# Kernel optimization log

Hardware: AMD Instinct MI355X
Metric: run time of the kernel (lower is better)

## Reference

```python
import jax, jax.numpy as jnp
import numpy as np

DQ = 256  # query feature size
DK = 256  # key feature size
DV = 256  # value feature size
B, SQ, SK = 4, 256, 256
D = DQ + DK  # MLP hidden width (512)


def setup_inputs() -> dict:
    key = jax.random.key(0)
    ks = jax.random.split(key, 7)
    Q = jax.random.normal(ks[0], (B, SQ, DQ), dtype=jnp.float32)
    K = jax.random.normal(ks[1], (B, SK, DK), dtype=jnp.float32)
    V = jax.random.normal(ks[2], (B, SK, DV), dtype=jnp.float32)
    # key-padding style mask: True = masked out. Keep at least the first key
    # unmasked so softmax rows are well-behaved.
    mask_out = jax.random.randint(ks[3], (B, 1, SK), 0, 2).astype(jnp.bool_)
    mask_out = mask_out.at[:, :, 0].set(False)
    # nn.Linear(D, D, bias=True): weight [D, D], bias [D]
    lim1 = 1.0 / np.sqrt(D)
    W1 = jax.random.uniform(ks[4], (D, D), minval=-lim1, maxval=lim1, dtype=jnp.float32)
    b1 = jax.random.uniform(ks[5], (D,), minval=-lim1, maxval=lim1, dtype=jnp.float32)
    # nn.Linear(D, 1, bias=False): weight [1, D] -> store as vector [D]
    W2 = jax.random.uniform(ks[6], (D,), minval=-lim1, maxval=lim1, dtype=jnp.float32)
    return {"Q": Q, "K": K, "V": V, "mask_out": mask_out, "W1": W1, "b1": b1, "W2": W2}


def reference(Q, K, V, mask_out, W1, b1, W2):
    # Concat-then-Linear splits: cat([q,k]) @ W1.T == q @ W1[:, :DQ].T + k @ W1[:, DQ:].T
    q_h = jnp.einsum('bqd,hd->bqh', Q, W1[:, :DQ])          # [B,SQ,D]
    k_h = jnp.einsum('bkd,hd->bkh', K, W1[:, DQ:])          # [B,SK,D]
    hidden = q_h[:, :, None, :] + k_h[:, None, :, :] + b1   # [B,SQ,SK,D]
    act = jax.nn.leaky_relu(hidden, negative_slope=0.01)
    scores = jnp.einsum('bqkh,h->bqk', act, W2)             # [B,SQ,SK]
    scores = jnp.where(mask_out, jnp.float32(-1e9), scores)
    attn = jax.nn.softmax(scores, axis=-1)
    return jnp.einsum('bqk,bkv->bqv', attn, V)              # [B,SQ,DV]
```

## Files before the change

kernel.cpp:

```cpp
#include <hip/hip_runtime.h>

#define HH_OFF 0
#define KT_OFF (1024 * 512)

typedef short short8 __attribute__((ext_vector_type(8)));
typedef float f32x4 __attribute__((ext_vector_type(4)));

union S8 {
  short8 v;
  unsigned short s[8];
};

__device__ __forceinline__ unsigned bf16rne(float x) {
  unsigned u = __float_as_uint(x);
  u += 0x7FFFu + ((u >> 16) & 1u);
  return u >> 16;
}

__device__ __forceinline__ void cvt_split8(const float4& f0, const float4& f1,
                                           short8& hv8, short8& lv8) {
  float xs[8] = {f0.x, f0.y, f0.z, f0.w, f1.x, f1.y, f1.z, f1.w};
  S8 hv, lv;
#pragma unroll
  for (int e = 0; e < 8; ++e) {
    unsigned u = __float_as_uint(xs[e]);
    unsigned hu = u & 0xFFFF0000u;
    hv.s[e] = (unsigned short)(hu >> 16);
    float lo = xs[e] - __uint_as_float(hu);
    unsigned ul = __float_as_uint(lo);
    ul += 0x7FFFu + ((ul >> 16) & 1u);
    lv.s[e] = (unsigned short)(ul >> 16);
  }
  hv8 = hv.v;
  lv8 = lv.v;
}

__global__ __launch_bounds__(512) void gemm_k(const float* __restrict__ Q,
                                              const float* __restrict__ Kin,
                                              const float* __restrict__ W1,
                                              const float* __restrict__ b1,
                                              float* __restrict__ hh,
                                              unsigned* __restrict__ kT2) {
  __shared__ short AH[64 * 32], AL[64 * 32], BH[64 * 32], BL[64 * 32];
  const int t = threadIdx.x;
  const int blk = blockIdx.x;
  const bool isK = blk >= 128;
  const float *A, *B;
  int lda, ldb, m0, n0, aoff;
  if (!isK) {
    int bm = blk >> 3, bn = blk & 7;
    m0 = bm * 64; n0 = bn * 64;
    A = Q;   lda = 256; aoff = 0;
    B = W1;  ldb = 512;
  } else {
    int t2 = blk - 128;
    int bm = t2 >> 4, bn = t2 & 15;
    m0 = bm * 64; n0 = bn * 64;
    A = W1;  lda = 512; aoff = 256;
    B = Kin; ldb = 256;
  }
  const int mat = t >> 8;
  const int cc = t & 255;
  const int sr = cc >> 2;
  const int c8 = (cc & 3) * 8;
  const float* srcbase =
      mat ? (B + (size_t)(n0 + sr) * ldb + c8)
          : (A + (size_t)(m0 + sr) * lda + aoff + c8);
  short* dstH = (mat ? BH : AH) + sr * 32 + c8;
  short* dstL = (mat ? BL : AL) + sr * 32 + c8;

  const int w = t >> 6, lane = t & 63;
  const int wr = (w >> 2) * 32, wc = (w & 3) * 16;
  const int lane15 = lane & 15, lk8 = (lane >> 4) * 8;

  f32x4 acc[2] = {{0.f, 0.f, 0.f, 0.f}, {0.f, 0.f, 0.f, 0.f}};

  float4 f0 = *(const float4*)&srcbase[0];
  float4 f1 = *(const float4*)&srcbase[4];
  for (int ks = 0; ks < 8; ++ks) {
    short8 hv8, lv8;
    cvt_split8(f0, f1, hv8, lv8);
    __syncthreads();
    *(short8*)dstH = hv8;
    *(short8*)dstL = lv8;
    __syncthreads();
    if (ks < 7) {
      f0 = *(const float4*)&srcbase[(ks + 1) * 32];
      f1 = *(const float4*)&srcbase[(ks + 1) * 32 + 4];
    }
    short8 ah0 = *(const short8*)&AH[(wr + lane15) * 32 + lk8];
    short8 ah1 = *(const short8*)&AH[(wr + 16 + lane15) * 32 + lk8];
    short8 al0 = *(const short8*)&AL[(wr + lane15) * 32 + lk8];
    short8 al1 = *(const short8*)&AL[(wr + 16 + lane15) * 32 + lk8];
    short8 bh = *(const short8*)&BH[(wc + lane15) * 32 + lk8];
    short8 bl = *(const short8*)&BL[(wc + lane15) * 32 + lk8];
    acc[0] = __builtin_amdgcn_mfma_f32_16x16x32_bf16(ah0, bh, acc[0], 0, 0, 0);
    acc[1] = __builtin_amdgcn_mfma_f32_16x16x32_bf16(ah1, bh, acc[1], 0, 0, 0);
    acc[0] = __builtin_amdgcn_mfma_f32_16x16x32_bf16(ah0, bl, acc[0], 0, 0, 0);
    acc[1] = __builtin_amdgcn_mfma_f32_16x16x32_bf16(ah1, bl, acc[1], 0, 0, 0);
    acc[0] = __builtin_amdgcn_mfma_f32_16x16x32_bf16(al0, bh, acc[0], 0, 0, 0);
    acc[1] = __builtin_amdgcn_mfma_f32_16x16x32_bf16(al1, bh, acc[1], 0, 0, 0);
  }
  const int lg4 = (lane >> 4) * 4;
  if (!isK) {
#pragma unroll
    for (int i = 0; i < 2; ++i) {
#pragma unroll
      for (int reg = 0; reg < 4; ++reg) {
        int row = m0 + wr + i * 16 + lg4 + reg;
        hh[(size_t)row * 512 + n0 + wc + lane15] = acc[i][reg];
      }
    }
  } else {
    const int col = n0 + wc + lane15;
#pragma unroll
    for (int i = 0; i < 2; ++i) {
      int r0 = m0 + wr + i * 16 + lg4;
      float v0 = acc[i][0] + b1[r0 + 0];
      float v1 = acc[i][1] + b1[r0 + 1];
      float v2 = acc[i][2] + b1[r0 + 2];
      float v3 = acc[i][3] + b1[r0 + 3];
      unsigned p01 = bf16rne(v0) | (bf16rne(v1) << 16);
      unsigned p23 = bf16rne(v2) | (bf16rne(v3) << 16);
      int hp = r0 >> 1;
      kT2[(size_t)hp * 1024 + col] = p01;
      kT2[(size_t)(hp + 1) * 1024 + col] = p23;
    }
  }
}

__global__ __launch_bounds__(512) void attn_k(const float* __restrict__ hh,
                                              const unsigned* __restrict__ kT2,
                                              const float* __restrict__ V,
                                              const void* __restrict__ maskp,
                                              const float* __restrict__ W2,
                                              float* __restrict__ out) {
  __shared__ float smem[14016];
  __shared__ int sflag, nkS;
  __shared__ int wsumS[4];
  __shared__ int kidxS[256];
  float* att = smem;
  float* rowsum = smem + 1040;
  float* qlin = smem + 1044;
  float* qs = smem + 1056;
  float* w2s = smem + 3104;
  float* sabs = smem + 3616;
  float* klin = smem + 11936;
  float* red = smem + 3616;

  const int t = threadIdx.x;
  const int blk = blockIdx.x;
  const int b = blk >> 6;
  const int q4 = blk & 63;
  const int w = t >> 6, lane = t & 63;

  if (t == 0) sflag = 0;
  {
    const float* qbase = hh + (size_t)(b * 256 + q4 * 4) * 512;
    int row = t >> 7, c4 = (t & 127) * 4;
    *(float4*)&qs[row * 512 + c4] = *(const float4*)&qbase[(size_t)row * 512 + c4];
    if (t < 128) *(float4*)&w2s[t * 4] = *(const float4*)&W2[t * 4];
  }
  __syncthreads();
  if (t < 256) {
    const unsigned char* mb = (const unsigned char*)maskp;
    int nz = mb[t * 4 + 1] | mb[t * 4 + 2] | mb[t * 4 + 3];
    if (nz) atomicOr(&sflag, 1);
  }
  if (w < 4) {
    float p = 0.f;
#pragma unroll
    for (int u = 0; u < 8; ++u)
      p = fmaf(w2s[lane + 64 * u], qs[w * 512 + lane + 64 * u], p);
#pragma unroll
    for (int o = 32; o; o >>= 1) p += __shfl_xor(p, o, 64);
    if (lane == 0) qlin[w] = 0.505f * p;
  }
  __syncthreads();
  bool act = false;
  int pre = 0;
  if (t < 256) {
    const int flag = sflag;
    const unsigned char* m8 = (const unsigned char*)maskp;
    const int* m32 = (const int*)maskp;
    act = flag ? (m8[b * 256 + t] == 0) : (m32[b * 256 + t] == 0);
    unsigned long long bal = __ballot(act);
    pre = __popcll(bal & ((1ull << lane) - 1ull));
    if (lane == 0) wsumS[w] = __popcll(bal);
  }
  __syncthreads();
  if (t < 256 && act) {
    int off = 0;
#pragma unroll
    for (int ww = 0; ww < 4; ++ww)
      if (ww < w) off += wsumS[ww];
    kidxS[off + pre] = t;
  }
  if (t == 0) nkS = wsumS[0] + wsumS[1] + wsumS[2] + wsumS[3];
  __syncthreads();
  const int nk = nkS;
  const int ncg = (nk + 63) >> 6;

  {
    float sa[4][4] = {};
    float kl[4] = {};
    const unsigned* kTbase = kT2 + (size_t)b * 256;
    const unsigned* colp[4];
#pragma unroll
    for (int cg = 0; cg < 4; ++cg) {
      int ci = cg * 64 + lane;
      int kc = kidxS[ci < nk ? ci : (nk - 1)];
      colp[cg] = kTbase + kc;
    }
    const int hbase = w * 64;
#pragma unroll 2
    for (int hg = 0; hg < 16; ++hg) {
      const int h = hbase + hg * 4;
      const int hp = h >> 1;
      unsigned ua[4], ub[4];
#pragma unroll
      for (int cg = 0; cg < 4; ++cg)
        if (cg < ncg) {
          ua[cg] = colp[cg][(size_t)hp * 1024];
          ub[cg] = colp[cg][(size_t)(hp + 1) * 1024];
        }
      float w24[4], qv[4][4];
      *(float4*)w24 = *(const float4*)&w2s[h];
#pragma unroll
      for (int q = 0; q < 4; ++q)
        *(float4*)qv[q] = *(const float4*)&qs[q * 512 + h];
#pragma unroll
      for (int cg = 0; cg < 4; ++cg)
        if (cg < ncg) {
          float kv[4];
          kv[0] = __uint_as_float(ua[cg] << 16);
          kv[1] = __uint_as_float(ua[cg] & 0xFFFF0000u);
          kv[2] = __uint_as_float(ub[cg] << 16);
          kv[3] = __uint_as_float(ub[cg] & 0xFFFF0000u);
#pragma unroll
          for (int e = 0; e < 4; ++e) {
            kl[cg] = fmaf(w24[e], kv[e], kl[cg]);
#pragma unroll
            for (int q = 0; q < 4; ++q)
              sa[q][cg] = fmaf(w24[e], fabsf(qv[q][e] + kv[e]), sa[q][cg]);
          }
        }
    }
#pragma unroll
    for (int cg = 0; cg < 4; ++cg)
      if (cg < ncg) {
        int ci = cg * 64 + lane;
#pragma unroll
        for (int q = 0; q < 4; ++q) sabs[(w * 4 + q) * 260 + ci] = sa[q][cg];
        klin[w * 260 + ci] = kl[cg];
      }
  }
  __syncthreads();
  if (t < 256) {
#pragma unroll
    for (int q = 0; q < 4; ++q) att[q * 260 + t] = -1e9f;
  }
  __syncthreads();
  if (t < nk) {
    const int realk = kidxS[t];
    float kls = 0.f;
#pragma unroll
    for (int ww = 0; ww < 8; ++ww) kls += klin[ww * 260 + t];
    kls *= 0.505f;
#pragma unroll
    for (int q = 0; q < 4; ++q) {
      float v = 0.f;
#pragma unroll
      for (int ww = 0; ww < 8; ++ww) v += sabs[(ww * 4 + q) * 260 + t];
      att[q * 260 + realk] = qlin[q] + kls + 0.495f * v;
    }
  }
  __syncthreads();
  if (w < 4) {
    float m = -1e30f;
#pragma unroll
    for (int u = 0; u < 4; ++u) m = fmaxf(m, att[w * 260 + lane + 64 * u]);
#pragma unroll
    for (int o = 32; o; o >>= 1) m = fmaxf(m, __shfl_xor(m, o, 64));
    float ssum = 0.f;
#pragma unroll
    for (int u = 0; u < 4; ++u) {
      float e = __expf(att[w * 260 + lane + 64 * u] - m);
      att[w * 260 + lane + 64 * u] = e;
      ssum += e;
    }
#pragma unroll
    for (int o = 32; o; o >>= 1) ssum += __shfl_xor(ssum, o, 64);
    if (lane == 0) rowsum[w] = ssum;
  }
  __syncthreads();
  {
    const int v0 = lane * 4;
    const float* Vb = V + (size_t)b * 65536;
    float acc[4][4] = {};
    for (int i = w; i < nk; i += 8) {
      int k = kidxS[i];
      float4 vv = *(const float4*)&Vb[(size_t)k * 256 + v0];
      float aw[4];
#pragma unroll
      for (int q = 0; q < 4; ++q) aw[q] = att[q * 260 + k];
#pragma unroll
      for (int q = 0; q < 4; ++q) {
        acc[q][0] = fmaf(aw[q], vv.x, acc[q][0]);
        acc[q][1] = fmaf(aw[q], vv.y, acc[q][1]);
        acc[q][2] = fmaf(aw[q], vv.z, acc[q][2]);
        acc[q][3] = fmaf(aw[q], vv.w, acc[q][3]);
      }
    }
#pragma unroll
    for (int q = 0; q < 4; ++q)
      *(float4*)&red[(w * 4 + q) * 264 + v0] =
          make_float4(acc[q][0], acc[q][1], acc[q][2], acc[q][3]);
  }
  __syncthreads();
#pragma unroll
  for (int s = 0; s < 2; ++s) {
    int id = t + s * 512;
    int row = id >> 8, col = id & 255;
    float v = 0.f;
#pragma unroll
    for (int g = 0; g < 8; ++g) v += red[(g * 4 + row) * 264 + col];
    out[((size_t)b * 256 + q4 * 4 + row) * 256 + col] = v / rowsum[row];
  }
}

extern "C" void kernel_launch(void* const* d_in, const int* in_sizes, int n_in,
                              void* d_out, int out_size, void* d_ws,
                              size_t ws_size, hipStream_t stream) {
  const float* Q = (const float*)d_in[0];
  const float* K = (const float*)d_in[1];
  const float* V = (const float*)d_in[2];
  const void* mask = d_in[3];
  const float* W1 = (const float*)d_in[4];
  const float* b1 = (const float*)d_in[5];
  const float* W2 = (const float*)d_in[6];
  float* ws = (float*)d_ws;
  float* hh = ws + HH_OFF;
  unsigned* kT2 = (unsigned*)(ws + KT_OFF);
  float* out = (float*)d_out;

  gemm_k<<<dim3(256), dim3(512), 0, stream>>>(Q, K, W1, b1, hh, kT2);
  attn_k<<<dim3(256), dim3(512), 0, stream>>>(hh, kT2, V, mask, W2, out);
}
```

Baseline: 34.76 us.

## Compact unmasked keys in GEMM stage and vectorize packed key reads in attention

The K-projection blocks now build the list of unmasked keys for their batch, skip column chunks with no surviving keys, and gather K rows in compacted order. kT2 therefore holds only unmasked columns contiguously. The attention kernel reads them with 128-bit loads over 4 adjacent columns per lane, splits the hidden dimension across lane gangs, and combines the partial sums with cross-lane shuffles. This removes the per-lane indirect gather and masked-key work, at the cost of mask scanning and extra barriers in the GEMM blocks.

Result: faster. 30.28 us (-12.9%).

```diff
diff --git a/kernel.cpp b/kernel.cpp
--- a/kernel.cpp
+++ b/kernel.cpp
@@ -39,14 +39,16 @@
                                               const float* __restrict__ Kin,
                                               const float* __restrict__ W1,
                                               const float* __restrict__ b1,
+                                              const void* __restrict__ maskp,
                                               float* __restrict__ hh,
                                               unsigned* __restrict__ kT2) {
   __shared__ short AH[64 * 32], AL[64 * 32], BH[64 * 32], BL[64 * 32];
+  __shared__ int sflag, nkS, wsumS[4], kidxS[256];
   const int t = threadIdx.x;
   const int blk = blockIdx.x;
   const bool isK = blk >= 128;
   const float *A, *B;
-  int lda, ldb, m0, n0, aoff;
+  int lda, ldb, m0, n0, aoff, bb = 0, cchunk = 0;
   if (!isK) {
     int bm = blk >> 3, bn = blk & 7;
     m0 = bm * 64; n0 = bn * 64;
@@ -58,14 +60,53 @@
     m0 = bm * 64; n0 = bn * 64;
     A = W1;  lda = 512; aoff = 256;
     B = Kin; ldb = 256;
+    bb = bn >> 2; cchunk = bn & 3;
+    if (t == 0) sflag = 0;
+    __syncthreads();
+    if (t < 256) {
+      const unsigned char* mb = (const unsigned char*)maskp;
+      int nz = mb[t * 4 + 1] | mb[t * 4 + 2] | mb[t * 4 + 3];
+      if (nz) atomicOr(&sflag, 1);
+    }
+    __syncthreads();
+    const int w_ = t >> 6, lane_ = t & 63;
+    bool act = false;
+    int pre = 0;
+    if (t < 256) {
+      const int flag = sflag;
+      const unsigned char* m8 = (const unsigned char*)maskp;
+      const int* m32 = (const int*)maskp;
+      act = flag ? (m8[bb * 256 + t] == 0) : (m32[bb * 256 + t] == 0);
+      unsigned long long bal = __ballot(act);
+      pre = __popcll(bal & ((1ull << lane_) - 1ull));
+      if (lane_ == 0) wsumS[w_] = __popcll(bal);
+    }
+    __syncthreads();
+    if (t < 256 && act) {
+      int off = 0;
+#pragma unroll
+      for (int ww = 0; ww < 4; ++ww)
+        if (ww < w_) off += wsumS[ww];
+      kidxS[off + pre] = t;
+    }
+    if (t == 0) nkS = wsumS[0] + wsumS[1] + wsumS[2] + wsumS[3];
+    __syncthreads();
+    if (cchunk * 64 >= ((nkS + 63) & ~63)) return;
   }
   const int mat = t >> 8;
   const int cc = t & 255;
   const int sr = cc >> 2;
   const int c8 = (cc & 3) * 8;
-  const float* srcbase =
-      mat ? (B + (size_t)(n0 + sr) * ldb + c8)
-          : (A + (size_t)(m0 + sr) * lda + aoff + c8);
+  const float* srcbase;
+  if (mat == 0) {
+    srcbase = A + (size_t)(m0 + sr) * lda + aoff + c8;
+  } else if (!isK) {
+    srcbase = B + (size_t)(n0 + sr) * ldb + c8;
+  } else {
+    int jl = cchunk * 64 + sr;
+    int kr = kidxS[jl < nkS ? jl : nkS - 1];
+    srcbase = Kin + (size_t)(bb * 256 + kr) * 256 + c8;
+  }
   short* dstH = (mat ? BH : AH) + sr * 32 + c8;
   short* dstL = (mat ? BL : AL) + sr * 32 + c8;
 
@@ -136,8 +177,7 @@
                                               const float* __restrict__ W2,
                                               float* __restrict__ out) {
   __shared__ float smem[14016];
-  __shared__ int sflag, nkS;
-  __shared__ int wsumS[4];
+  __shared__ int sflag, nkS, wsumS[4];
   __shared__ int kidxS[256];
   float* att = smem;
   float* rowsum = smem + 1040;
@@ -199,61 +239,70 @@
   if (t == 0) nkS = wsumS[0] + wsumS[1] + wsumS[2] + wsumS[3];
   __syncthreads();
   const int nk = nkS;
-  const int ncg = (nk + 63) >> 6;
+  const int nc64 = (nk + 63) >> 6;
 
   {
-    float sa[4][4] = {};
-    float kl[4] = {};
-    const unsigned* kTbase = kT2 + (size_t)b * 256;
-    const unsigned* colp[4];
-#pragma unroll
-    for (int cg = 0; cg < 4; ++cg) {
-      int ci = cg * 64 + lane;
-      int kc = kidxS[ci < nk ? ci : (nk - 1)];
-      colp[cg] = kTbase + kc;
-    }
-    const int hbase = w * 64;
-#pragma unroll 2
-    for (int hg = 0; hg < 16; ++hg) {
-      const int h = hbase + hg * 4;
-      const int hp = h >> 1;
-      unsigned ua[4], ub[4];
-#pragma unroll
-      for (int cg = 0; cg < 4; ++cg)
-        if (cg < ncg) {
-          ua[cg] = colp[cg][(size_t)hp * 1024];
-          ub[cg] = colp[cg][(size_t)(hp + 1) * 1024];
+    const int gang = lane >> 4, li = lane & 15;
+    const int hbase = w * 64 + gang * 16;
+    const unsigned* kTb = kT2 + (size_t)b * 256;
+#pragma unroll 1
+    for (int cb = 0; cb < nc64; ++cb) {
+      const int colo = cb * 64 + li * 4;
+      float sa[4][4] = {};
+      float kl4[4] = {};
+#pragma unroll
+      for (int hg = 0; hg < 4; ++hg) {
+        const int h = hbase + hg * 4;
+        const int hp = h >> 1;
+        uint4 ua = *(const uint4*)&kTb[(size_t)hp * 1024 + colo];
+        uint4 ub = *(const uint4*)&kTb[(size_t)(hp + 1) * 1024 + colo];
+        float w24[4], qv[4][4];
+        *(float4*)w24 = *(const float4*)&w2s[h];
+#pragma unroll
+        for (int q = 0; q < 4; ++q)
+          *(float4*)qv[q] = *(const float4*)&qs[q * 512 + h];
+        unsigned uac[4] = {ua.x, ua.y, ua.z, ua.w};
+        unsigned ubc[4] = {ub.x, ub.y, ub.z, ub.w};
+        float kv[4][4];
+#pragma unroll
+        for (int c = 0; c < 4; ++c) {
+          kv[0][c] = __uint_as_float(uac[c] << 16);
+          kv[1][c] = __uint_as_float(uac[c] & 0xFFFF0000u);
+          kv[2][c] = __uint_as_float(ubc[c] << 16);
+          kv[3][c] = __uint_as_float(ubc[c] & 0xFFFF0000u);
         }
-      float w24[4], qv[4][4];
-      *(float4*)w24 = *(const float4*)&w2s[h];
-#pragma unroll
-      for (int q = 0; q < 4; ++q)
-        *(float4*)qv[q] = *(const float4*)&qs[q * 512 + h];
-#pragma unroll
-      for (int cg = 0; cg < 4; ++cg)
-        if (cg < ncg) {
-          float kv[4];
-          kv[0] = __uint_as_float(ua[cg] << 16);
-          kv[1] = __uint_as_float(ua[cg] & 0xFFFF0000u);
-          kv[2] = __uint_as_float(ub[cg] << 16);
-          kv[3] = __uint_as_float(ub[cg] & 0xFFFF0000u);
-#pragma unroll
-          for (int e = 0; e < 4; ++e) {
-            kl[cg] = fmaf(w24[e], kv[e], kl[cg]);
+#pragma unroll
+        for (int e = 0; e < 4; ++e) {
+#pragma unroll
+          for (int c = 0; c < 4; ++c) {
+            kl4[c] = fmaf(w24[e], kv[e][c], kl4[c]);
 #pragma unroll
             for (int q = 0; q < 4; ++q)
-              sa[q][cg] = fmaf(w24[e], fabsf(qv[q][e] + kv[e]), sa[q][cg]);
+              sa[q][c] = fmaf(w24[e], fabsf(qv[q][e] + kv[e][c]), sa[q][c]);
           }
         }
-    }
-#pragma unroll
-    for (int cg = 0; cg < 4; ++cg)
-      if (cg < ncg) {
-        int ci = cg * 64 + lane;
-#pragma unroll
-        for (int q = 0; q < 4; ++q) sabs[(w * 4 + q) * 260 + ci] = sa[q][cg];
-        klin[w * 260 + ci] = kl[cg];
-      }
+      }
+#pragma unroll
+      for (int q = 0; q < 4; ++q)
+#pragma unroll
+        for (int c = 0; c < 4; ++c) {
+          sa[q][c] += __shfl_xor(sa[q][c], 16, 64);
+          sa[q][c] += __shfl_xor(sa[q][c], 32, 64);
+        }
+#pragma unroll
+      for (int c = 0; c < 4; ++c) {
+        kl4[c] += __shfl_xor(kl4[c], 16, 64);
+        kl4[c] += __shfl_xor(kl4[c], 32, 64);
+      }
+      if (gang == 0) {
+#pragma unroll
+        for (int q = 0; q < 4; ++q)
+          *(float4*)&sabs[(w * 4 + q) * 260 + colo] =
+              make_float4(sa[q][0], sa[q][1], sa[q][2], sa[q][3]);
+        *(float4*)&klin[w * 260 + colo] =
+            make_float4(kl4[0], kl4[1], kl4[2], kl4[3]);
+      }
+    }
   }
   __syncthreads();
   if (t < 256) {
@@ -344,6 +393,6 @@
   unsigned* kT2 = (unsigned*)(ws + KT_OFF);
   float* out = (float*)d_out;
 
-  gemm_k<<<dim3(256), dim3(512), 0, stream>>>(Q, K, W1, b1, hh, kT2);
+  gemm_k<<<dim3(256), dim3(512), 0, stream>>>(Q, K, W1, b1, mask, hh, kT2);
   attn_k<<<dim3(256), dim3(512), 0, stream>>>(hh, kT2, V, mask, W2, out);
 }
```
